# Performance work log

Hardware: AMD Instinct MI355X
Metric: run time of the kernel (lower is better)

Reference implementation:

```python
import jax, jax.numpy as jnp
import numpy as np


def setup_inputs() -> dict:
    key = jax.random.key(0)
    k = jax.random.split(key, 7)
    B, IN, OUT = 128, 1024, 1024
    return {
        "x": jax.random.normal(k[0], (B, IN), dtype=jnp.float32),
        "eps": jax.random.normal(k[1], (B, IN, OUT), dtype=jnp.float32),
        "eps_bias": jax.random.normal(k[2], (B, OUT), dtype=jnp.float32),
        "mu": jax.random.normal(k[3], (IN, OUT), dtype=jnp.float32),
        "ro": jax.random.normal(k[4], (IN, OUT), dtype=jnp.float32),
        "mu_bias": jax.random.normal(k[5], (1, OUT), dtype=jnp.float32),
        "ro_bias": jax.random.normal(k[6], (1, OUT), dtype=jnp.float32),
    }


def reference(x, eps, eps_bias, mu, ro, mu_bias, ro_bias):
    # softplus: log(1 + exp(ro)) as written in the original module
    sigma = jnp.log1p(jnp.exp(ro))            # [in, out]
    sigma_bias = jnp.log1p(jnp.exp(ro_bias))  # [1, out]
    weights = eps * sigma + mu                # [B, in, out] per-sample weights
    bias = eps_bias * sigma_bias + mu_bias    # [B, out]
    # (x.unsqueeze(1) @ weights).squeeze() -> per-sample matvec
    return jnp.einsum("bi,bio->bo", x, weights) + bias
```

## Files before the change

### kernel.cpp

```cpp
#include <hip/hip_runtime.h>
#include <math.h>

#define BB 128
#define IN 1024
#define OUTD 1024
#define ISPLIT 16
#define ICHUNK (IN / ISPLIT)

typedef float f4v __attribute__((ext_vector_type(4)));

__device__ __forceinline__ float softplus(float r) {
    return fmaxf(r, 0.0f) + log1pf(expf(-fabsf(r)));
}

__global__ __launch_bounds__(256) void prep_sigma(const float* __restrict__ ro,
                                                  float* __restrict__ sigma) {
    int idx = blockIdx.x * 256 + threadIdx.x;
    float4 r = ((const float4*)ro)[idx];
    float4 s;
    s.x = softplus(r.x);
    s.y = softplus(r.y);
    s.z = softplus(r.z);
    s.w = softplus(r.w);
    ((float4*)sigma)[idx] = s;
}

__global__ __launch_bounds__(256, 4) void bayes_main(
    const float* __restrict__ x, const float* __restrict__ eps,
    const float* __restrict__ mu, const float* __restrict__ sigma,
    float* __restrict__ partial) {
    __shared__ float xs[8][ICHUNK];
    const int tid = threadIdx.x;

    const int bid = blockIdx.x;
    const int xcd = bid & 7;
    const int t = bid >> 3;
    const int s_local = t & 7;
    const int bblk = t >> 3;
    const int slice = s_local * 8 + xcd;
    const int oblk = slice & 3;
    const int iblk = slice >> 2;
    const int b0 = bblk * 8;
    const int o0 = oblk * 256;
    const int i0 = iblk * ICHUNK;

    for (int tt = tid; tt < 8 * ICHUNK; tt += 256) {
        int bb = tt / ICHUNK, ii = tt % ICHUNK;
        xs[bb][ii] = x[(size_t)(b0 + bb) * IN + i0 + ii];
    }
    __syncthreads();

    const int oq = tid & 63;
    const int bsub = tid >> 6;
    const int o = o0 + oq * 4;

    const float4* sp = (const float4*)(sigma + (size_t)i0 * OUTD + o);
    const float4* mp = (const float4*)(mu + (size_t)i0 * OUTD + o);
    const f4v* e0p = (const f4v*)(eps + ((size_t)(b0 + bsub) * IN + i0) * OUTD + o);
    const f4v* e1p =
        (const f4v*)(eps + ((size_t)(b0 + 4 + bsub) * IN + i0) * OUTD + o);

    float4 acc0 = {0.f, 0.f, 0.f, 0.f};
    float4 acc1 = {0.f, 0.f, 0.f, 0.f};

#pragma unroll 4
    for (int ii = 0; ii < ICHUNK; ++ii) {
        float4 s = sp[(size_t)ii * (OUTD / 4)];
        float4 m = mp[(size_t)ii * (OUTD / 4)];
        f4v e0 = __builtin_nontemporal_load(e0p + (size_t)ii * (OUTD / 4));
        f4v e1 = __builtin_nontemporal_load(e1p + (size_t)ii * (OUTD / 4));
        float x0 = xs[bsub][ii];
        float x1 = xs[bsub + 4][ii];
        acc0.x = fmaf(x0, fmaf(e0.x, s.x, m.x), acc0.x);
        acc0.y = fmaf(x0, fmaf(e0.y, s.y, m.y), acc0.y);
        acc0.z = fmaf(x0, fmaf(e0.z, s.z, m.z), acc0.z);
        acc0.w = fmaf(x0, fmaf(e0.w, s.w, m.w), acc0.w);
        acc1.x = fmaf(x1, fmaf(e1.x, s.x, m.x), acc1.x);
        acc1.y = fmaf(x1, fmaf(e1.y, s.y, m.y), acc1.y);
        acc1.z = fmaf(x1, fmaf(e1.z, s.z, m.z), acc1.z);
        acc1.w = fmaf(x1, fmaf(e1.w, s.w, m.w), acc1.w);
    }

    float* pp0 = partial + ((size_t)iblk * BB + (b0 + bsub)) * OUTD + o;
    *(float4*)pp0 = acc0;
    float* pp1 = partial + ((size_t)iblk * BB + (b0 + 4 + bsub)) * OUTD + o;
    *(float4*)pp1 = acc1;
}

__global__ __launch_bounds__(256) void finalize(
    const float* __restrict__ partial, const float* __restrict__ eps_bias,
    const float* __restrict__ mu_bias, const float* __restrict__ ro_bias,
    float* __restrict__ out) {
    int idx = blockIdx.x * 256 + threadIdx.x;
    int p = idx * 4;
    int o = p & (OUTD - 1);

    float4 acc = {0.f, 0.f, 0.f, 0.f};
#pragma unroll
    for (int is = 0; is < ISPLIT; ++is) {
        float4 a = *(const float4*)(partial + (size_t)is * BB * OUTD + p);
        acc.x += a.x;
        acc.y += a.y;
        acc.z += a.z;
        acc.w += a.w;
    }
    float4 eb = *(const float4*)(eps_bias + p);
    float4 rb = *(const float4*)(ro_bias + o);
    float4 mb = *(const float4*)(mu_bias + o);

    float4 r;
    r.x = acc.x + eb.x * softplus(rb.x) + mb.x;
    r.y = acc.y + eb.y * softplus(rb.y) + mb.y;
    r.z = acc.z + eb.z * softplus(rb.z) + mb.z;
    r.w = acc.w + eb.w * softplus(rb.w) + mb.w;
    ((float4*)out)[idx] = r;
}

extern "C" void kernel_launch(void* const* d_in, const int* in_sizes, int n_in,
                              void* d_out, int out_size, void* d_ws, size_t ws_size,
                              hipStream_t stream) {
    const float* x = (const float*)d_in[0];
    const float* eps = (const float*)d_in[1];
    const float* eps_bias = (const float*)d_in[2];
    const float* mu = (const float*)d_in[3];
    const float* ro = (const float*)d_in[4];
    const float* mu_bias = (const float*)d_in[5];
    const float* ro_bias = (const float*)d_in[6];
    float* out = (float*)d_out;

    float* sigma = (float*)d_ws;
    float* partial = sigma + (size_t)IN * OUTD;

    prep_sigma<<<(IN * OUTD / 4) / 256, 256, 0, stream>>>(ro, sigma);

    bayes_main<<<1024, 256, 0, stream>>>(x, eps, mu, sigma, partial);

    finalize<<<(BB * OUTD / 4) / 256, 256, 0, stream>>>(partial, eps_bias, mu_bias,
                                                        ro_bias, out);
}
```

Measured before the change: 105.0 us.

## Process 16 batches per block and interleave sigma/mu into one buffer

Each block now covers 16 batch rows instead of 8, so every sigma/mu value loaded is reused across four eps streams per thread. The grid is halved and occupancy hints drop to 2 blocks per CU. Sigma and mu are also packed side by side in the prep kernel so the main loop reads them from one interleaved buffer. The main cost targeted is repeated sigma/mu traffic. In exchange the workspace doubles, the prep kernel does an extra copy of mu, and with fewer blocks and more registers per thread there is less parallelism to hide the dominant eps streaming.

```diff
diff --git a/kernel.cpp b/kernel.cpp
--- a/kernel.cpp
+++ b/kernel.cpp
@@ -13,23 +13,25 @@
     return fmaxf(r, 0.0f) + log1pf(expf(-fabsf(r)));
 }
 
-__global__ __launch_bounds__(256) void prep_sigma(const float* __restrict__ ro,
-                                                  float* __restrict__ sigma) {
+__global__ __launch_bounds__(256) void prep_sm(const float* __restrict__ ro,
+                                               const float* __restrict__ mu,
+                                               float* __restrict__ sm) {
     int idx = blockIdx.x * 256 + threadIdx.x;
     float4 r = ((const float4*)ro)[idx];
+    float4 m = ((const float4*)mu)[idx];
     float4 s;
     s.x = softplus(r.x);
     s.y = softplus(r.y);
     s.z = softplus(r.z);
     s.w = softplus(r.w);
-    ((float4*)sigma)[idx] = s;
+    ((float4*)sm)[idx * 2] = s;
+    ((float4*)sm)[idx * 2 + 1] = m;
 }
 
-__global__ __launch_bounds__(256, 4) void bayes_main(
+__global__ __launch_bounds__(256, 2) void bayes_main(
     const float* __restrict__ x, const float* __restrict__ eps,
-    const float* __restrict__ mu, const float* __restrict__ sigma,
-    float* __restrict__ partial) {
-    __shared__ float xs[8][ICHUNK];
+    const float* __restrict__ sm, float* __restrict__ partial) {
+    __shared__ float xs[16][ICHUNK];
     const int tid = threadIdx.x;
 
     const int bid = blockIdx.x;
@@ -40,11 +42,11 @@
     const int slice = s_local * 8 + xcd;
     const int oblk = slice & 3;
     const int iblk = slice >> 2;
-    const int b0 = bblk * 8;
+    const int b0 = bblk * 16;
     const int o0 = oblk * 256;
     const int i0 = iblk * ICHUNK;
 
-    for (int tt = tid; tt < 8 * ICHUNK; tt += 256) {
+    for (int tt = tid; tt < 16 * ICHUNK; tt += 256) {
         int bb = tt / ICHUNK, ii = tt % ICHUNK;
         xs[bb][ii] = x[(size_t)(b0 + bb) * IN + i0 + ii];
     }
@@ -54,23 +56,33 @@
     const int bsub = tid >> 6;
     const int o = o0 + oq * 4;
 
-    const float4* sp = (const float4*)(sigma + (size_t)i0 * OUTD + o);
-    const float4* mp = (const float4*)(mu + (size_t)i0 * OUTD + o);
-    const f4v* e0p = (const f4v*)(eps + ((size_t)(b0 + bsub) * IN + i0) * OUTD + o);
+    const float4* smp = (const float4*)(sm + ((size_t)i0 * OUTD + o) * 2);
+    const f4v* e0p =
+        (const f4v*)(eps + ((size_t)(b0 + bsub) * IN + i0) * OUTD + o);
     const f4v* e1p =
-        (const f4v*)(eps + ((size_t)(b0 + 4 + bsub) * IN + i0) * OUTD + o);
+        (const f4v*)(eps + ((size_t)(b0 + bsub + 4) * IN + i0) * OUTD + o);
+    const f4v* e2p =
+        (const f4v*)(eps + ((size_t)(b0 + bsub + 8) * IN + i0) * OUTD + o);
+    const f4v* e3p =
+        (const f4v*)(eps + ((size_t)(b0 + bsub + 12) * IN + i0) * OUTD + o);
 
     float4 acc0 = {0.f, 0.f, 0.f, 0.f};
     float4 acc1 = {0.f, 0.f, 0.f, 0.f};
+    float4 acc2 = {0.f, 0.f, 0.f, 0.f};
+    float4 acc3 = {0.f, 0.f, 0.f, 0.f};
 
 #pragma unroll 4
     for (int ii = 0; ii < ICHUNK; ++ii) {
-        float4 s = sp[(size_t)ii * (OUTD / 4)];
-        float4 m = mp[(size_t)ii * (OUTD / 4)];
+        float4 s = smp[(size_t)ii * (OUTD / 2)];
+        float4 m = smp[(size_t)ii * (OUTD / 2) + 1];
         f4v e0 = __builtin_nontemporal_load(e0p + (size_t)ii * (OUTD / 4));
         f4v e1 = __builtin_nontemporal_load(e1p + (size_t)ii * (OUTD / 4));
+        f4v e2 = __builtin_nontemporal_load(e2p + (size_t)ii * (OUTD / 4));
+        f4v e3 = __builtin_nontemporal_load(e3p + (size_t)ii * (OUTD / 4));
         float x0 = xs[bsub][ii];
         float x1 = xs[bsub + 4][ii];
+        float x2 = xs[bsub + 8][ii];
+        float x3 = xs[bsub + 12][ii];
         acc0.x = fmaf(x0, fmaf(e0.x, s.x, m.x), acc0.x);
         acc0.y = fmaf(x0, fmaf(e0.y, s.y, m.y), acc0.y);
         acc0.z = fmaf(x0, fmaf(e0.z, s.z, m.z), acc0.z);
@@ -79,12 +91,21 @@
         acc1.y = fmaf(x1, fmaf(e1.y, s.y, m.y), acc1.y);
         acc1.z = fmaf(x1, fmaf(e1.z, s.z, m.z), acc1.z);
         acc1.w = fmaf(x1, fmaf(e1.w, s.w, m.w), acc1.w);
+        acc2.x = fmaf(x2, fmaf(e2.x, s.x, m.x), acc2.x);
+        acc2.y = fmaf(x2, fmaf(e2.y, s.y, m.y), acc2.y);
+        acc2.z = fmaf(x2, fmaf(e2.z, s.z, m.z), acc2.z);
+        acc2.w = fmaf(x2, fmaf(e2.w, s.w, m.w), acc2.w);
+        acc3.x = fmaf(x3, fmaf(e3.x, s.x, m.x), acc3.x);
+        acc3.y = fmaf(x3, fmaf(e3.y, s.y, m.y), acc3.y);
+        acc3.z = fmaf(x3, fmaf(e3.z, s.z, m.z), acc3.z);
+        acc3.w = fmaf(x3, fmaf(e3.w, s.w, m.w), acc3.w);
     }
 
-    float* pp0 = partial + ((size_t)iblk * BB + (b0 + bsub)) * OUTD + o;
-    *(float4*)pp0 = acc0;
-    float* pp1 = partial + ((size_t)iblk * BB + (b0 + 4 + bsub)) * OUTD + o;
-    *(float4*)pp1 = acc1;
+    float* base = partial + ((size_t)iblk * BB) * OUTD + o;
+    *(float4*)(base + (size_t)(b0 + bsub) * OUTD) = acc0;
+    *(float4*)(base + (size_t)(b0 + bsub + 4) * OUTD) = acc1;
+    *(float4*)(base + (size_t)(b0 + bsub + 8) * OUTD) = acc2;
+    *(float4*)(base + (size_t)(b0 + bsub + 12) * OUTD) = acc3;
 }
 
 __global__ __launch_bounds__(256) void finalize(
@@ -128,12 +149,12 @@
     const float* ro_bias = (const float*)d_in[6];
     float* out = (float*)d_out;
 
-    float* sigma = (float*)d_ws;
-    float* partial = sigma + (size_t)IN * OUTD;
+    float* sm = (float*)d_ws;
+    float* partial = sm + (size_t)2 * IN * OUTD;
 
-    prep_sigma<<<(IN * OUTD / 4) / 256, 256, 0, stream>>>(ro, sigma);
+    prep_sm<<<(IN * OUTD / 4) / 256, 256, 0, stream>>>(ro, mu, sm);
 
-    bayes_main<<<1024, 256, 0, stream>>>(x, eps, mu, sigma, partial);
+    bayes_main<<<512, 256, 0, stream>>>(x, eps, sm, partial);
 
     finalize<<<(BB * OUTD / 4) / 256, 256, 0, stream>>>(partial, eps_bias, mu_bias,
                                                         ro_bias, out);
```

Result: no change. 104.3 us (-0.6%).
